# Optimization experiments

Measured on AMD Instinct MI355X. Metric: run time of the kernel, lower is better.

The kernel has to match this reference:

```python
import jax, jax.numpy as jnp
import numpy as np

NEG_SLOPE = 0.2  # GATv2Conv default negative_slope
EPS = 1e-5       # BatchNorm1d default eps


def _bn(x, g, b):
    # training-mode batch norm (biased variance, matching torch normalization)
    m = x.mean(0)
    v = x.var(0)
    return (x - m) / jnp.sqrt(v + EPS) * g + b


def setup_inputs() -> dict:
    key = jax.random.key(0)
    N, E, AIN, EIN, HID, H, OUT = 50000, 400000, 64, 16, 64, 8, 1
    ks = jax.random.split(key, 16)
    def nrm(k, shape, s=0.05):
        return jax.random.normal(k, shape, jnp.float32) * s
    return dict(
        x=nrm(ks[0], (N, AIN), 1.0),
        edge_index=jax.random.randint(ks[1], (2, E), 0, N),
        edge_attr=nrm(ks[2], (E, EIN), 1.0),
        W_ap=nrm(ks[3], (AIN, HID)), b_ap=jnp.zeros((HID,), jnp.float32),
        W_ep=nrm(ks[4], (EIN, HID)), b_ep=jnp.zeros((HID,), jnp.float32),
        W_msg=nrm(ks[5], (HID, HID)), b_msg=jnp.zeros((HID,), jnp.float32),
        g_msg=jnp.ones((HID,), jnp.float32), be_msg=jnp.zeros((HID,), jnp.float32),
        W_l=nrm(ks[6], (2 * HID, H * HID)), W_r=nrm(ks[7], (2 * HID, H * HID)),
        att=nrm(ks[8], (H, HID)), b_gat=jnp.zeros((H * HID,), jnp.float32),
        g_bn=jnp.ones((H * HID,), jnp.float32), be_bn=jnp.zeros((H * HID,), jnp.float32),
        W_p1=nrm(ks[9], (H * HID, HID)), b_p1=jnp.zeros((HID,), jnp.float32),
        g_p=jnp.ones((HID,), jnp.float32), be_p=jnp.zeros((HID,), jnp.float32),
        W_p2=nrm(ks[10], (HID, OUT)), b_p2=jnp.zeros((OUT,), jnp.float32),
    )


def reference(x, edge_index, edge_attr,
              W_ap, b_ap, W_ep, b_ep, W_msg, b_msg, g_msg, be_msg,
              W_l, W_r, att, b_gat, g_bn, be_bn,
              W_p1, b_p1, g_p, be_p, W_p2, b_p2):
    N = x.shape[0]
    H, C = att.shape
    row, col = edge_index[0], edge_index[1]

    atom = x @ W_ap + b_ap                      # [N, HID]
    ef = edge_attr @ W_ep + b_ep                # [E, HID]

    # scatter_mean of edge features onto destination nodes
    s = jax.ops.segment_sum(ef, col, num_segments=N)
    cnt = jax.ops.segment_sum(jnp.ones((ef.shape[0],), ef.dtype), col, num_segments=N)
    agg = s / jnp.clip(cnt, 1.0)[:, None]       # [N, HID]

    msg = jax.nn.relu(_bn((atom + agg) @ W_msg + b_msg, g_msg, be_msg))
    comb = jnp.concatenate([msg, agg], axis=1)  # [N, 2*HID]

    # GATv2Conv with default add_self_loops=True, concat=True
    src = jnp.concatenate([row, jnp.arange(N, dtype=row.dtype)])
    dst = jnp.concatenate([col, jnp.arange(N, dtype=col.dtype)])
    xl = (comb @ W_l).reshape(N, H, C)          # source transform
    xr = (comb @ W_r).reshape(N, H, C)          # target transform
    e = jax.nn.leaky_relu(xl[src] + xr[dst], NEG_SLOPE)   # [E+N, H, C]
    score = jnp.einsum('ehc,hc->eh', e, att)               # [E+N, H]
    smax = jax.ops.segment_max(score, dst, num_segments=N)
    ex = jnp.exp(score - smax[dst])
    denom = jax.ops.segment_sum(ex, dst, num_segments=N)
    alpha = ex / denom[dst]                                 # per-dst softmax
    out = jax.ops.segment_sum(alpha[:, :, None] * xl[src], dst, num_segments=N)
    out = out.reshape(N, H * C) + b_gat                     # [N, H*C]

    out = jax.nn.relu(_bn(out, g_bn, be_bn))
    h = jax.nn.relu(_bn(out @ W_p1 + b_p1, g_p, be_p))
    return (h @ W_p2 + b_p2).squeeze(-1)                    # [N]
```

## Files before the change

### kernel.cpp

```cpp
#include <hip/hip_runtime.h>
#include <hip/hip_bf16.h>


#define CDIV(a, b) (((a) + (b) - 1) / (b))

using f32x4 = __attribute__((ext_vector_type(4))) float;
using s16x8 = __attribute__((ext_vector_type(8))) short;

__device__ inline unsigned short f2bf(float f) {
    union { float f; unsigned u; } v; v.f = f;
    unsigned r = v.u + 0x7fff + ((v.u >> 16) & 1);
    return (unsigned short)(r >> 16);
}
__device__ inline float bf_lo(unsigned w) {
    union { unsigned u; float f; } v; v.u = w << 16; return v.f;
}
__device__ inline float bf_hi(unsigned w) {
    union { unsigned u; float f; } v; v.u = w & 0xffff0000u; return v.f;
}

__global__ void k_scatter16(const float* __restrict__ EA, const int* __restrict__ ei,
                            float* __restrict__ agg16, int* __restrict__ cntI, int E) {
    int t = blockIdx.x * blockDim.x + threadIdx.x;
    int e = t >> 4, ch = t & 15;
    if (e >= E) return;
    int dst = ei[E + e];
    atomicAdd(&agg16[(size_t)dst * 16 + ch], EA[(size_t)e * 16 + ch]);
    if (ch == 0) atomicAdd(&cntI[dst], 1);
}

__global__ void k_wc(const float* __restrict__ Wap, const float* __restrict__ Wmsg,
                     const float* __restrict__ bap, const float* __restrict__ bmsg,
                     unsigned short* __restrict__ Wzt, float* __restrict__ bc) {
    int t = threadIdx.x;
    for (int e = t; e < 4096; e += 256) {
        int i = e >> 6, c = e & 63;
        float s = 0.f;
        for (int j = 0; j < 64; ++j) s += Wap[i * 64 + j] * Wmsg[j * 64 + c];
        Wzt[c * 128 + i] = f2bf(s);
    }
    for (int e = t; e < 4096; e += 256) {
        int k = e >> 6, c = e & 63;
        Wzt[c * 128 + 64 + k] = f2bf(Wmsg[k * 64 + c]);
    }
    if (t < 64) {
        float s = bmsg[t];
        for (int j = 0; j < 64; ++j) s += bap[j] * Wmsg[j * 64 + t];
        bc[t] = s;
    }
}

__global__ void k_xbf(const float* __restrict__ x, unsigned short* __restrict__ combin, int N) {
    int idx = blockIdx.x * blockDim.x + threadIdx.x;
    if (idx >= N * 64) return;
    int n = idx >> 6, k = idx & 63;
    combin[(size_t)n * 128 + k] = f2bf(x[idx]);
}

__global__ void k_aggfin(const float* __restrict__ agg16, const int* __restrict__ cntI,
                         const float* __restrict__ Wep, const float* __restrict__ bep,
                         unsigned short* __restrict__ combin, int N) {
    int wid = (blockIdx.x * blockDim.x + threadIdx.x) >> 6;
    int lane = threadIdx.x & 63;
    if (wid >= N) return;
    int c = cntI[wid];
    float mval = (lane < 16 && c > 0) ? agg16[(size_t)wid * 16 + lane] / (float)c : 0.f;
    float acc = bep[lane];
#pragma unroll
    for (int j = 0; j < 16; ++j) {
        float mj = __shfl(mval, j, 64);
        acc = fmaf(mj, Wep[j * 64 + lane], acc);
    }
    if (c == 0) acc = 0.f;
    combin[(size_t)wid * 128 + 64 + lane] = f2bf(acc);
}

__global__ __launch_bounds__(256) void k_z(
    const unsigned short* __restrict__ combin, const unsigned short* __restrict__ Wzt,
    const float* __restrict__ bc, float* __restrict__ z, float* __restrict__ sums, int N) {
    __shared__ unsigned short a_lds[64 * 128];
    __shared__ unsigned short b_lds[64 * 128];
    __shared__ float redS[64], redQ[64];
    int t = threadIdx.x;
    int row0 = blockIdx.x * 64;
    for (int i = t; i < 1024; i += 256) {
        int row = i >> 4, seg = i & 15;
        int dsts = (row * 256 + ((seg * 16) ^ ((row & 7) << 4))) >> 1;
        int gr = row0 + row;
        s16x8 v = (s16x8)0;
        if (gr < N) v = *(const s16x8*)(combin + (size_t)gr * 128 + seg * 8);
        *(s16x8*)(a_lds + dsts) = v;
        *(s16x8*)(b_lds + dsts) = *(const s16x8*)(Wzt + (size_t)row * 128 + seg * 8);
    }
    if (t < 64) { redS[t] = 0.f; redQ[t] = 0.f; }
    __syncthreads();
    int w = t >> 6, l = t & 63, hi = l >> 4, lo = l & 15;
    int ar = w * 16 + lo;
    s16x8 a[4];
#pragma unroll
    for (int kk = 0; kk < 4; ++kk) {
        int byte = (kk * 64 + hi * 16) ^ ((ar & 7) << 4);
        a[kk] = *(const s16x8*)(a_lds + ((ar * 256 + byte) >> 1));
    }
#pragma unroll
    for (int cf = 0; cf < 4; ++cf) {
        int br = cf * 16 + lo;
        f32x4 acc = (f32x4){0.f, 0.f, 0.f, 0.f};
#pragma unroll
        for (int kk = 0; kk < 4; ++kk) {
            int byte = (kk * 64 + hi * 16) ^ ((br & 7) << 4);
            s16x8 b = *(const s16x8*)(b_lds + ((br * 256 + byte) >> 1));
            acc = __builtin_amdgcn_mfma_f32_16x16x32_bf16(a[kk], b, acc, 0, 0, 0);
        }
        int colg = cf * 16 + lo;
        float bcv = bc[colg];
        float sv = 0.f, qv = 0.f;
#pragma unroll
        for (int r = 0; r < 4; ++r) {
            int rowg = row0 + w * 16 + hi * 4 + r;
            if (rowg < N) {
                float v = acc[r] + bcv;
                z[(size_t)rowg * 64 + colg] = v;
                sv += v; qv += v * v;
            }
        }
        atomicAdd(&redS[colg], sv);
        atomicAdd(&redQ[colg], qv);
    }
    __syncthreads();
    if (t < 64) {
        atomicAdd(&sums[t], redS[t]);
        atomicAdd(&sums[64 + t], redQ[t]);
    }
}

__global__ __launch_bounds__(256) void k_statsg(const uint4* __restrict__ X,
                                                float* __restrict__ sums, int N) {
    __shared__ float redS[512], redQ[512];
    int t = threadIdx.x;
    for (int i = t; i < 512; i += 256) { redS[i] = 0.f; redQ[i] = 0.f; }
    __syncthreads();
    int qu = t & 63;
    int slice = (blockIdx.x << 2) | (t >> 6);
    int nsl = gridDim.x << 2;
    float s[8], q[8];
#pragma unroll
    for (int j = 0; j < 8; ++j) { s[j] = 0.f; q[j] = 0.f; }
    for (int n = slice; n < N; n += nsl) {
        uint4 u = X[(size_t)n * 64 + qu];
        unsigned uu[4] = {u.x, u.y, u.z, u.w};
#pragma unroll
        for (int k2 = 0; k2 < 4; ++k2) {
            float a = bf_lo(uu[k2]), b = bf_hi(uu[k2]);
            s[2 * k2] += a; q[2 * k2] += a * a;
            s[2 * k2 + 1] += b; q[2 * k2 + 1] += b * b;
        }
    }
#pragma unroll
    for (int j = 0; j < 8; ++j) {
        atomicAdd(&redS[qu * 8 + j], s[j]);
        atomicAdd(&redQ[qu * 8 + j], q[j]);
    }
    __syncthreads();
    for (int i = t; i < 512; i += 256) {
        atomicAdd(&sums[i], redS[i]);
        atomicAdd(&sums[512 + i], redQ[i]);
    }
}

__global__ void k_bnparam(const float* __restrict__ sums, const float* __restrict__ g,
                          const float* __restrict__ be, float* __restrict__ sc,
                          float* __restrict__ sh, int N) {
    int k = blockIdx.x * blockDim.x + threadIdx.x;
    if (k >= 512) return;
    float invN = 1.0f / (float)N;
    float mean = sums[k] * invN;
    float var = sums[512 + k] * invN - mean * mean;
    float s = g[k] * rsqrtf(var + 1e-5f);
    sc[k] = s;
    sh[k] = be[k] - mean * s;
}

__global__ void k_comb2(const float* __restrict__ z, const float* __restrict__ stats,
                        const float* __restrict__ g, const float* __restrict__ be,
                        unsigned short* __restrict__ combin, int N) {
    int idx = blockIdx.x * blockDim.x + threadIdx.x;
    if (idx >= N * 64) return;
    int n = idx >> 6, k = idx & 63;
    float invN = 1.0f / (float)N;
    float mean = stats[k] * invN;
    float var = stats[64 + k] * invN - mean * mean;
    float inv = rsqrtf(var + 1e-5f);
    float v = fmaxf((z[idx] - mean) * (inv * g[k]) + be[k], 0.f);
    combin[(size_t)n * 128 + k] = f2bf(v);
}

__global__ void k_bsum(const int* __restrict__ cntI, int* __restrict__ bsum, int N) {
    int b = blockIdx.x, t = threadIdx.x;
    int base = b * 1024 + t * 4;
    int s = 0;
#pragma unroll
    for (int j = 0; j < 4; ++j) { int i = base + j; if (i < N) s += cntI[i]; }
    for (int off = 32; off; off >>= 1) s += __shfl_xor(s, off, 64);
    __shared__ int wsum[4];
    if ((t & 63) == 0) wsum[t >> 6] = s;
    __syncthreads();
    if (t == 0) bsum[b] = wsum[0] + wsum[1] + wsum[2] + wsum[3];
}
__global__ void k_boff(const int* __restrict__ bsum, int* __restrict__ boff, int nb) {
    int t = threadIdx.x;
    if (t < nb) { int s = 0; for (int j = 0; j < t; ++j) s += bsum[j]; boff[t] = s; }
}
__global__ void k_scan2(const int* __restrict__ cntI, const int* __restrict__ boff,
                        int* __restrict__ rowptr, int N) {
    int b = blockIdx.x, t = threadIdx.x;
    int base = b * 1024 + t * 4;
    int v[4]; int s = 0;
#pragma unroll
    for (int j = 0; j < 4; ++j) { int i = base + j; v[j] = (i < N) ? cntI[i] : 0; s += v[j]; }
    __shared__ int ls[256];
    ls[t] = s; __syncthreads();
    for (int off = 1; off < 256; off <<= 1) {
        int tv = (t >= (int)off) ? ls[t - off] : 0;
        __syncthreads(); ls[t] += tv; __syncthreads();
    }
    int run = ls[t] - s + boff[b];
#pragma unroll
    for (int j = 0; j < 4; ++j) { run += v[j]; int i = base + j; if (i < N) rowptr[i + 1] = run; }
    if (b == 0 && t == 0) rowptr[0] = 0;
}

__global__ void k_fill(const int* __restrict__ ei, const int* __restrict__ rowptr,
                       int* __restrict__ cursor, int* __restrict__ esrc, int E) {
    int e = blockIdx.x * blockDim.x + threadIdx.x;
    if (e >= E) return;
    int dst = ei[E + e];
    int pos = rowptr[dst] + atomicAdd(&cursor[dst], 1);
    esrc[pos] = ei[e];
}

__global__ void k_prep_w(const float* __restrict__ Wl, const float* __restrict__ Wr,
                         unsigned short* __restrict__ Wt) {
    int idx = blockIdx.x * blockDim.x + threadIdx.x;
    if (idx >= 1024 * 128) return;
    int c = idx >> 7, k = idx & 127;
    float v = (c < 512) ? Wl[(size_t)k * 512 + c] : Wr[(size_t)k * 512 + (c - 512)];
    Wt[idx] = f2bf(v);
}

__global__ void k_prep_w1(const float* __restrict__ Wp1, unsigned short* __restrict__ Wp1t) {
    int idx = blockIdx.x * blockDim.x + threadIdx.x;
    if (idx >= 64 * 512) return;
    int c = idx >> 9, k = idx & 511;
    Wp1t[idx] = f2bf(Wp1[(size_t)k * 64 + c]);
}

__global__ __launch_bounds__(256) void k_xlxr2(
    const unsigned short* __restrict__ combin, const unsigned short* __restrict__ Wt,
    unsigned short* __restrict__ xlr, int N) {
    __shared__ unsigned short a_lds[64 * 128];
    __shared__ unsigned short b_lds[256 * 128];
    int t = threadIdx.x;
    int row0 = blockIdx.x * 64;
    int c0 = blockIdx.y * 256;
    for (int i = t; i < 1024; i += 256) {
        int row = i >> 4, seg = i & 15;
        int dsts = (row * 256 + ((seg * 16) ^ ((row & 7) << 4))) >> 1;
        int gr = row0 + row;
        s16x8 v = (s16x8)0;
        if (gr < N) v = *(const s16x8*)(combin + (size_t)gr * 128 + seg * 8);
        *(s16x8*)(a_lds + dsts) = v;
    }
    for (int i = t; i < 4096; i += 256) {
        int row = i >> 4, seg = i & 15;
        int dsts = (row * 256 + ((seg * 16) ^ ((row & 7) << 4))) >> 1;
        *(s16x8*)(b_lds + dsts) = *(const s16x8*)(Wt + (size_t)(c0 + row) * 128 + seg * 8);
    }
    __syncthreads();
    int w = t >> 6, l = t & 63, hi = l >> 4, lo = l & 15;
    int ar = w * 16 + lo;
    s16x8 a[4];
#pragma unroll
    for (int kk = 0; kk < 4; ++kk) {
        int byte = (kk * 64 + hi * 16) ^ ((ar & 7) << 4);
        a[kk] = *(const s16x8*)(a_lds + ((ar * 256 + byte) >> 1));
    }
#pragma unroll
    for (int cf = 0; cf < 16; ++cf) {
        int br = cf * 16 + lo;
        f32x4 acc = (f32x4){0.f, 0.f, 0.f, 0.f};
#pragma unroll
        for (int kk = 0; kk < 4; ++kk) {
            int byte = (kk * 64 + hi * 16) ^ ((br & 7) << 4);
            s16x8 b = *(const s16x8*)(b_lds + ((br * 256 + byte) >> 1));
            acc = __builtin_amdgcn_mfma_f32_16x16x32_bf16(a[kk], b, acc, 0, 0, 0);
        }
        int colg = c0 + cf * 16 + lo;
#pragma unroll
        for (int r = 0; r < 4; ++r) {
            int rowg = row0 + w * 16 + hi * 4 + r;
            if (rowg < N) xlr[(size_t)rowg * 1024 + colg] = f2bf(acc[r]);
        }
    }
}

__global__ __launch_bounds__(256) void k_gat(
    const unsigned short* __restrict__ xlr, unsigned* __restrict__ gout32,
    const int* __restrict__ rowptr, const int* __restrict__ esrc,
    const float* __restrict__ att, const float* __restrict__ bg, int N) {
    int wid = (blockIdx.x * blockDim.x + threadIdx.x) >> 6;
    int lane = threadIdx.x & 63;
    if (wid >= N) return;
    int n = wid;
    float xrv[8], av[8], acc[8];
    {
        uint4 u = *(const uint4*)(xlr + (size_t)n * 1024 + 512 + lane * 8);
        xrv[0] = bf_lo(u.x); xrv[1] = bf_hi(u.x); xrv[2] = bf_lo(u.y); xrv[3] = bf_hi(u.y);
        xrv[4] = bf_lo(u.z); xrv[5] = bf_hi(u.z); xrv[6] = bf_lo(u.w); xrv[7] = bf_hi(u.w);
    }
#pragma unroll
    for (int j = 0; j < 8; ++j) { av[j] = att[lane * 8 + j]; acc[j] = 0.f; }
    float m = -1e30f, s = 0.f;
    int e0 = rowptr[n], e1 = rowptr[n + 1];
    for (int e = e0; e <= e1; ++e) {
        int src = (e < e1) ? esrc[e] : n;
        uint4 u = *(const uint4*)(xlr + (size_t)src * 1024 + lane * 8);
        float xlv[8] = {bf_lo(u.x), bf_hi(u.x), bf_lo(u.y), bf_hi(u.y),
                        bf_lo(u.z), bf_hi(u.z), bf_lo(u.w), bf_hi(u.w)};
        float ps = 0.f;
#pragma unroll
        for (int j = 0; j < 8; ++j) {
            float tv = xlv[j] + xrv[j];
            tv = (tv > 0.f) ? tv : 0.2f * tv;
            ps = fmaf(tv, av[j], ps);
        }
        ps += __shfl_xor(ps, 1, 64);
        ps += __shfl_xor(ps, 2, 64);
        ps += __shfl_xor(ps, 4, 64);
        float mnew = fmaxf(m, ps);
        float sc = __expf(m - mnew);
        float w = __expf(ps - mnew);
        s = s * sc + w;
#pragma unroll
        for (int j = 0; j < 8; ++j) acc[j] = acc[j] * sc + w * xlv[j];
        m = mnew;
    }
    float invs = 1.0f / s;
    unsigned o[4];
#pragma unroll
    for (int p = 0; p < 4; ++p) {
        float lo = acc[2 * p] * invs + bg[lane * 8 + 2 * p];
        float hi = acc[2 * p + 1] * invs + bg[lane * 8 + 2 * p + 1];
        o[p] = (unsigned)f2bf(lo) | ((unsigned)f2bf(hi) << 16);
    }
    *(uint4*)(gout32 + (size_t)n * 256 + lane * 4) = make_uint4(o[0], o[1], o[2], o[3]);
}

__global__ __launch_bounds__(256) void k_postm(
    const unsigned* __restrict__ gout32, const unsigned short* __restrict__ Wp1t,
    const float* __restrict__ sc, const float* __restrict__ sh,
    const float* __restrict__ bp1, float* __restrict__ h1, float* __restrict__ sums,
    int N) {
    __shared__ unsigned short a_lds[64 * 128];
    __shared__ unsigned short b_lds[64 * 128];
    __shared__ float sc_l[512], sh_l[512];
    __shared__ float redS[64], redQ[64];
    int t = threadIdx.x;
    for (int i = t; i < 512; i += 256) { sc_l[i] = sc[i]; sh_l[i] = sh[i]; }
    if (t < 64) { redS[t] = 0.f; redQ[t] = 0.f; }
    int row0 = blockIdx.x * 64;
    int w = t >> 6, l = t & 63, hi = l >> 4, lo = l & 15;
    int ar = w * 16 + lo;
    f32x4 acc[4];
#pragma unroll
    for (int cf = 0; cf < 4; ++cf) acc[cf] = (f32x4){0.f, 0.f, 0.f, 0.f};
    for (int kc = 0; kc < 4; ++kc) {
        __syncthreads();
        for (int i = t; i < 1024; i += 256) {
            int row = i >> 4, seg = i & 15;
            int dsts = (row * 256 + ((seg * 16) ^ ((row & 7) << 4))) >> 1;
            int gr = row0 + row;
            int k0 = kc * 128 + seg * 8;
            s16x8 v = (s16x8)0;
            if (gr < N) {
                uint4 u = *(const uint4*)(gout32 + (size_t)gr * 256 + (k0 >> 1));
                float f[8] = {bf_lo(u.x), bf_hi(u.x), bf_lo(u.y), bf_hi(u.y),
                              bf_lo(u.z), bf_hi(u.z), bf_lo(u.w), bf_hi(u.w)};
#pragma unroll
                for (int j = 0; j < 8; ++j) {
                    float y = fmaxf(fmaf(f[j], sc_l[k0 + j], sh_l[k0 + j]), 0.f);
                    v[j] = (short)f2bf(y);
                }
            }
            *(s16x8*)(a_lds + dsts) = v;
            *(s16x8*)(b_lds + dsts) = *(const s16x8*)(Wp1t + (size_t)row * 512 + k0);
        }
        __syncthreads();
        s16x8 a[4];
#pragma unroll
        for (int kk = 0; kk < 4; ++kk) {
            int byte = (kk * 64 + hi * 16) ^ ((ar & 7) << 4);
            a[kk] = *(const s16x8*)(a_lds + ((ar * 256 + byte) >> 1));
        }
#pragma unroll
        for (int cf = 0; cf < 4; ++cf) {
            int br = cf * 16 + lo;
#pragma unroll
            for (int kk = 0; kk < 4; ++kk) {
                int byte = (kk * 64 + hi * 16) ^ ((br & 7) << 4);
                s16x8 b = *(const s16x8*)(b_lds + ((br * 256 + byte) >> 1));
                acc[cf] = __builtin_amdgcn_mfma_f32_16x16x32_bf16(a[kk], b, acc[cf], 0, 0, 0);
            }
        }
    }
#pragma unroll
    for (int cf = 0; cf < 4; ++cf) {
        int colg = cf * 16 + lo;
        float bv = bp1[colg];
        float sv = 0.f, qv = 0.f;
#pragma unroll
        for (int r = 0; r < 4; ++r) {
            int rowg = row0 + w * 16 + hi * 4 + r;
            if (rowg < N) {
                float v = acc[cf][r] + bv;
                h1[(size_t)rowg * 64 + colg] = v;
                sv += v; qv += v * v;
            }
        }
        atomicAdd(&redS[colg], sv);
        atomicAdd(&redQ[colg], qv);
    }
    __syncthreads();
    if (t < 64) {
        atomicAdd(&sums[t], redS[t]);
        atomicAdd(&sums[64 + t], redQ[t]);
    }
}

__global__ void k_final(const float* __restrict__ h1, const float* __restrict__ stats,
                        const float* __restrict__ g, const float* __restrict__ be,
                        const float* __restrict__ Wp2, const float* __restrict__ bp2,
                        float* __restrict__ out, int N) {
    int wid = (blockIdx.x * blockDim.x + threadIdx.x) >> 6;
    int lane = threadIdx.x & 63;
    if (wid >= N) return;
    float invN = 1.0f / (float)N;
    float mean = stats[lane] * invN;
    float var = stats[64 + lane] * invN - mean * mean;
    float inv = rsqrtf(var + 1e-5f);
    float v = h1[(size_t)wid * 64 + lane];
    v = fmaxf((v - mean) * (inv * g[lane]) + be[lane], 0.f);
    float p = v * Wp2[lane];
#pragma unroll
    for (int off = 32; off; off >>= 1) p += __shfl_xor(p, off, 64);
    if (lane == 0) out[wid] = p + bp2[0];
}

extern "C" void kernel_launch(void* const* d_in, const int* in_sizes, int n_in,
                              void* d_out, int out_size, void* d_ws, size_t ws_size,
                              hipStream_t stream) {
    const float* x      = (const float*)d_in[0];
    const int*   ei     = (const int*)d_in[1];
    const float* ea     = (const float*)d_in[2];
    const float* W_ap   = (const float*)d_in[3];
    const float* b_ap   = (const float*)d_in[4];
    const float* W_ep   = (const float*)d_in[5];
    const float* b_ep   = (const float*)d_in[6];
    const float* W_msg  = (const float*)d_in[7];
    const float* b_msg  = (const float*)d_in[8];
    const float* g_msg  = (const float*)d_in[9];
    const float* be_msg = (const float*)d_in[10];
    const float* W_l    = (const float*)d_in[11];
    const float* W_r    = (const float*)d_in[12];
    const float* att    = (const float*)d_in[13];
    const float* b_gat  = (const float*)d_in[14];
    const float* g_bn   = (const float*)d_in[15];
    const float* be_bn  = (const float*)d_in[16];
    const float* W_p1   = (const float*)d_in[17];
    const float* b_p1   = (const float*)d_in[18];
    const float* g_p    = (const float*)d_in[19];
    const float* be_p   = (const float*)d_in[20];
    const float* W_p2   = (const float*)d_in[21];
    const float* b_p2   = (const float*)d_in[22];

    int N = in_sizes[0] / 64;
    int E = in_sizes[1] / 2;
    int nb = CDIV(N, 1024);

    float* ws = (float*)d_ws;
    size_t off = 0;
    float* agg16  = ws + off; off += (size_t)N * 16;
    int*   cntI   = (int*)(ws + off); off += N;
    int*   cursor = (int*)(ws + off); off += N;
    float* st_msg = ws + off; off += 128;
    float* st_gat = ws + off; off += 1024;
    float* st_p   = ws + off; off += 128;
    size_t zero_floats = off;
    float* bn_sc  = ws + off; off += 512;
    float* bn_sh  = ws + off; off += 512;
    unsigned short* combin = (unsigned short*)(ws + off); off += (size_t)N * 64;
    float* zb     = ws + off; off += (size_t)N * 64;
    unsigned short* Wzt = (unsigned short*)(ws + off); off += 4096;
    float* bc     = ws + off; off += 64;
    int*   rowptr = (int*)(ws + off); off += (size_t)(N + 1); off = (off + 3) & ~(size_t)3;
    int*   esrc   = (int*)(ws + off); off += E;
    int*   bsum   = (int*)(ws + off); off += 64;
    int*   boff   = (int*)(ws + off); off += 64;
    unsigned short* Wt  = (unsigned short*)(ws + off); off += 65536;
    unsigned short* Wp1t = (unsigned short*)(ws + off); off += 16384;
    unsigned short* xlr = (unsigned short*)(ws + off); off += (size_t)N * 512;
    unsigned* gout32 = (unsigned*)(ws + off); off += (size_t)N * 256;
    float* h1 = zb;

    hipMemsetAsync(d_ws, 0, zero_floats * sizeof(float), stream);

    k_prep_w<<<CDIV(1024 * 128, 256), 256, 0, stream>>>(W_l, W_r, Wt);
    k_prep_w1<<<CDIV(64 * 512, 256), 256, 0, stream>>>(W_p1, Wp1t);
    k_wc<<<1, 256, 0, stream>>>(W_ap, W_msg, b_ap, b_msg, Wzt, bc);
    k_xbf<<<CDIV(N * 64, 256), 256, 0, stream>>>(x, combin, N);
    k_scatter16<<<CDIV(E * 16, 256), 256, 0, stream>>>(ea, ei, agg16, cntI, E);
    k_aggfin<<<CDIV(N * 64, 256), 256, 0, stream>>>(agg16, cntI, W_ep, b_ep, combin, N);
    k_z<<<CDIV(N, 64), 256, 0, stream>>>(combin, Wzt, bc, zb, st_msg, N);
    k_comb2<<<CDIV(N * 64, 256), 256, 0, stream>>>(zb, st_msg, g_msg, be_msg, combin, N);
    k_bsum<<<nb, 256, 0, stream>>>(cntI, bsum, N);
    k_boff<<<1, 64, 0, stream>>>(bsum, boff, nb);
    k_scan2<<<nb, 256, 0, stream>>>(cntI, boff, rowptr, N);
    k_fill<<<CDIV(E, 256), 256, 0, stream>>>(ei, rowptr, cursor, esrc, E);
    dim3 gx(CDIV(N, 64), 4);
    k_xlxr2<<<gx, 256, 0, stream>>>(combin, Wt, xlr, N);
    k_gat<<<CDIV(N * 64, 256), 256, 0, stream>>>(xlr, gout32, rowptr, esrc, att, b_gat, N);
    k_statsg<<<256, 256, 0, stream>>>((const uint4*)gout32, st_gat, N);
    k_bnparam<<<2, 256, 0, stream>>>(st_gat, g_bn, be_bn, bn_sc, bn_sh, N);
    k_postm<<<CDIV(N, 64), 256, 0, stream>>>(gout32, Wp1t, bn_sc, bn_sh, b_p1, h1, st_p, N);
    k_final<<<CDIV(N * 64, 256), 256, 0, stream>>>(h1, st_p, g_p, be_p, W_p2, b_p2,
                                                   (float*)d_out, N);
}
```

Before: 407.6 us.

## Fuse combin prep, vectorize BN apply, drop softmax max tracking in GAT

Merges the x-to-bf16 and edge-aggregation finish kernels into one kernel that writes packed bf16 pairs. Message batch-norm parameters are now precomputed by a tiny kernel, and the apply kernel reads them with float4 loads and writes packed output. The GAT aggregation loop drops the running max and its rescaling, processes two edges per iteration, and computes leaky ReLU with an fabs form. Skipping the max subtraction removes serial exp work but could overflow if attention scores grow large.

```diff
diff --git a/kernel.cpp b/kernel.cpp
--- a/kernel.cpp
+++ b/kernel.cpp
@@ -17,6 +17,10 @@
 }
 __device__ inline float bf_hi(unsigned w) {
     union { unsigned u; float f; } v; v.u = w & 0xffff0000u; return v.f;
+}
+__device__ inline void unp8(uint4 u, float* v) {
+    v[0] = bf_lo(u.x); v[1] = bf_hi(u.x); v[2] = bf_lo(u.y); v[3] = bf_hi(u.y);
+    v[4] = bf_lo(u.z); v[5] = bf_hi(u.z); v[6] = bf_lo(u.w); v[7] = bf_hi(u.w);
 }
 
 __global__ void k_scatter16(const float* __restrict__ EA, const int* __restrict__ ei,
@@ -50,29 +54,31 @@
     }
 }
 
-__global__ void k_xbf(const float* __restrict__ x, unsigned short* __restrict__ combin, int N) {
-    int idx = blockIdx.x * blockDim.x + threadIdx.x;
-    if (idx >= N * 64) return;
-    int n = idx >> 6, k = idx & 63;
-    combin[(size_t)n * 128 + k] = f2bf(x[idx]);
-}
-
-__global__ void k_aggfin(const float* __restrict__ agg16, const int* __restrict__ cntI,
-                         const float* __restrict__ Wep, const float* __restrict__ bep,
-                         unsigned short* __restrict__ combin, int N) {
+__global__ void k_combin(const float* __restrict__ x, const float* __restrict__ agg16,
+                         const int* __restrict__ cntI, const float* __restrict__ Wep,
+                         const float* __restrict__ bep, unsigned* __restrict__ combin32,
+                         int N) {
     int wid = (blockIdx.x * blockDim.x + threadIdx.x) >> 6;
     int lane = threadIdx.x & 63;
     if (wid >= N) return;
     int c = cntI[wid];
     float mval = (lane < 16 && c > 0) ? agg16[(size_t)wid * 16 + lane] / (float)c : 0.f;
-    float acc = bep[lane];
+    float aggv = bep[lane];
 #pragma unroll
     for (int j = 0; j < 16; ++j) {
         float mj = __shfl(mval, j, 64);
-        acc = fmaf(mj, Wep[j * 64 + lane], acc);
-    }
-    if (c == 0) acc = 0.f;
-    combin[(size_t)wid * 128 + 64 + lane] = f2bf(acc);
+        aggv = fmaf(mj, Wep[j * 64 + lane], aggv);
+    }
+    if (c == 0) aggv = 0.f;
+    float xv = x[(size_t)wid * 64 + lane];
+    int i0 = (lane & 31) * 2;
+    float ax = __shfl(xv, i0, 64);
+    float bx = __shfl(xv, i0 + 1, 64);
+    float aa = __shfl(aggv, i0, 64);
+    float ba = __shfl(aggv, i0 + 1, 64);
+    float a = (lane < 32) ? ax : aa;
+    float b = (lane < 32) ? bx : ba;
+    combin32[(size_t)wid * 64 + lane] = (unsigned)f2bf(a) | ((unsigned)f2bf(b) << 16);
 }
 
 __global__ __launch_bounds__(256) void k_z(
@@ -170,29 +176,31 @@
 
 __global__ void k_bnparam(const float* __restrict__ sums, const float* __restrict__ g,
                           const float* __restrict__ be, float* __restrict__ sc,
-                          float* __restrict__ sh, int N) {
+                          float* __restrict__ sh, int N, int C) {
     int k = blockIdx.x * blockDim.x + threadIdx.x;
-    if (k >= 512) return;
+    if (k >= C) return;
     float invN = 1.0f / (float)N;
     float mean = sums[k] * invN;
-    float var = sums[512 + k] * invN - mean * mean;
+    float var = sums[C + k] * invN - mean * mean;
     float s = g[k] * rsqrtf(var + 1e-5f);
     sc[k] = s;
     sh[k] = be[k] - mean * s;
 }
 
-__global__ void k_comb2(const float* __restrict__ z, const float* __restrict__ stats,
-                        const float* __restrict__ g, const float* __restrict__ be,
-                        unsigned short* __restrict__ combin, int N) {
+__global__ void k_comb2(const float* __restrict__ z, const float* __restrict__ sc,
+                        const float* __restrict__ sh, unsigned* __restrict__ combin32,
+                        int N) {
     int idx = blockIdx.x * blockDim.x + threadIdx.x;
-    if (idx >= N * 64) return;
-    int n = idx >> 6, k = idx & 63;
-    float invN = 1.0f / (float)N;
-    float mean = stats[k] * invN;
-    float var = stats[64 + k] * invN - mean * mean;
-    float inv = rsqrtf(var + 1e-5f);
-    float v = fmaxf((z[idx] - mean) * (inv * g[k]) + be[k], 0.f);
-    combin[(size_t)n * 128 + k] = f2bf(v);
+    if (idx >= N * 16) return;
+    int n = idx >> 4, kq = idx & 15;
+    float4 zv = *(const float4*)(z + (size_t)n * 64 + kq * 4);
+    float v0 = fmaxf(fmaf(zv.x, sc[kq * 4 + 0], sh[kq * 4 + 0]), 0.f);
+    float v1 = fmaxf(fmaf(zv.y, sc[kq * 4 + 1], sh[kq * 4 + 1]), 0.f);
+    float v2 = fmaxf(fmaf(zv.z, sc[kq * 4 + 2], sh[kq * 4 + 2]), 0.f);
+    float v3 = fmaxf(fmaf(zv.w, sc[kq * 4 + 3], sh[kq * 4 + 3]), 0.f);
+    unsigned lo = (unsigned)f2bf(v0) | ((unsigned)f2bf(v1) << 16);
+    unsigned hi = (unsigned)f2bf(v2) | ((unsigned)f2bf(v3) << 16);
+    *(uint2*)(combin32 + (size_t)n * 64 + kq * 2) = make_uint2(lo, hi);
 }
 
 __global__ void k_bsum(const int* __restrict__ cntI, int* __restrict__ bsum, int N) {
@@ -315,35 +323,63 @@
     float xrv[8], av[8], acc[8];
     {
         uint4 u = *(const uint4*)(xlr + (size_t)n * 1024 + 512 + lane * 8);
-        xrv[0] = bf_lo(u.x); xrv[1] = bf_hi(u.x); xrv[2] = bf_lo(u.y); xrv[3] = bf_hi(u.y);
-        xrv[4] = bf_lo(u.z); xrv[5] = bf_hi(u.z); xrv[6] = bf_lo(u.w); xrv[7] = bf_hi(u.w);
+        unp8(u, xrv);
     }
 #pragma unroll
     for (int j = 0; j < 8; ++j) { av[j] = att[lane * 8 + j]; acc[j] = 0.f; }
-    float m = -1e30f, s = 0.f;
+    float s = 0.f;
     int e0 = rowptr[n], e1 = rowptr[n + 1];
-    for (int e = e0; e <= e1; ++e) {
-        int src = (e < e1) ? esrc[e] : n;
-        uint4 u = *(const uint4*)(xlr + (size_t)src * 1024 + lane * 8);
-        float xlv[8] = {bf_lo(u.x), bf_hi(u.x), bf_lo(u.y), bf_hi(u.y),
-                        bf_lo(u.z), bf_hi(u.z), bf_lo(u.w), bf_hi(u.w)};
-        float ps = 0.f;
+    int m = e1 - e0 + 1;
+    int i = 0;
+    for (; i + 2 <= m; i += 2) {
+        int ia = e0 + i, ib = e0 + i + 1;
+        int s0 = (ia < e1) ? esrc[ia] : n;
+        int s1 = (ib < e1) ? esrc[ib] : n;
+        uint4 u0 = *(const uint4*)(xlr + (size_t)s0 * 1024 + lane * 8);
+        uint4 u1 = *(const uint4*)(xlr + (size_t)s1 * 1024 + lane * 8);
+        float xlv0[8], xlv1[8];
+        unp8(u0, xlv0); unp8(u1, xlv1);
+        float ps0 = 0.f, ps1 = 0.f;
 #pragma unroll
         for (int j = 0; j < 8; ++j) {
-            float tv = xlv[j] + xrv[j];
-            tv = (tv > 0.f) ? tv : 0.2f * tv;
-            ps = fmaf(tv, av[j], ps);
-        }
-        ps += __shfl_xor(ps, 1, 64);
-        ps += __shfl_xor(ps, 2, 64);
-        ps += __shfl_xor(ps, 4, 64);
-        float mnew = fmaxf(m, ps);
-        float sc = __expf(m - mnew);
-        float w = __expf(ps - mnew);
-        s = s * sc + w;
-#pragma unroll
-        for (int j = 0; j < 8; ++j) acc[j] = acc[j] * sc + w * xlv[j];
-        m = mnew;
+            float t0 = xlv0[j] + xrv[j];
+            float t1 = xlv1[j] + xrv[j];
+            t0 = fmaf(0.4f, fabsf(t0), 0.6f * t0);
+            t1 = fmaf(0.4f, fabsf(t1), 0.6f * t1);
+            ps0 = fmaf(t0, av[j], ps0);
+            ps1 = fmaf(t1, av[j], ps1);
+        }
+        ps0 += __shfl_xor(ps0, 1, 64); ps1 += __shfl_xor(ps1, 1, 64);
+        ps0 += __shfl_xor(ps0, 2, 64); ps1 += __shfl_xor(ps1, 2, 64);
+        ps0 += __shfl_xor(ps0, 4, 64); ps1 += __shfl_xor(ps1, 4, 64);
+        float w0 = __expf(ps0), w1 = __expf(ps1);
+        s += w0 + w1;
+#pragma unroll
+        for (int j = 0; j < 8; ++j) {
+            acc[j] = fmaf(w0, xlv0[j], acc[j]);
+            acc[j] = fmaf(w1, xlv1[j], acc[j]);
+        }
+    }
+    if (i < m) {
+        int ia = e0 + i;
+        int s0 = (ia < e1) ? esrc[ia] : n;
+        uint4 u0 = *(const uint4*)(xlr + (size_t)s0 * 1024 + lane * 8);
+        float xlv0[8];
+        unp8(u0, xlv0);
+        float ps0 = 0.f;
+#pragma unroll
+        for (int j = 0; j < 8; ++j) {
+            float t0 = xlv0[j] + xrv[j];
+            t0 = fmaf(0.4f, fabsf(t0), 0.6f * t0);
+            ps0 = fmaf(t0, av[j], ps0);
+        }
+        ps0 += __shfl_xor(ps0, 1, 64);
+        ps0 += __shfl_xor(ps0, 2, 64);
+        ps0 += __shfl_xor(ps0, 4, 64);
+        float w0 = __expf(ps0);
+        s += w0;
+#pragma unroll
+        for (int j = 0; j < 8; ++j) acc[j] = fmaf(w0, xlv0[j], acc[j]);
     }
     float invs = 1.0f / s;
     unsigned o[4];
@@ -384,8 +420,8 @@
             s16x8 v = (s16x8)0;
             if (gr < N) {
                 uint4 u = *(const uint4*)(gout32 + (size_t)gr * 256 + (k0 >> 1));
-                float f[8] = {bf_lo(u.x), bf_hi(u.x), bf_lo(u.y), bf_hi(u.y),
-                              bf_lo(u.z), bf_hi(u.z), bf_lo(u.w), bf_hi(u.w)};
+                float f[8];
+                unp8(u, f);
 #pragma unroll
                 for (int j = 0; j < 8; ++j) {
                     float y = fmaxf(fmaf(f[j], sc_l[k0 + j], sh_l[k0 + j]), 0.f);
@@ -498,6 +534,8 @@
     size_t zero_floats = off;
     float* bn_sc  = ws + off; off += 512;
     float* bn_sh  = ws + off; off += 512;
+    float* bn_sc2 = ws + off; off += 64;
+    float* bn_sh2 = ws + off; off += 64;
     unsigned short* combin = (unsigned short*)(ws + off); off += (size_t)N * 64;
     float* zb     = ws + off; off += (size_t)N * 64;
     unsigned short* Wzt = (unsigned short*)(ws + off); off += 4096;
@@ -517,11 +555,13 @@
     k_prep_w<<<CDIV(1024 * 128, 256), 256, 0, stream>>>(W_l, W_r, Wt);
     k_prep_w1<<<CDIV(64 * 512, 256), 256, 0, stream>>>(W_p1, Wp1t);
     k_wc<<<1, 256, 0, stream>>>(W_ap, W_msg, b_ap, b_msg, Wzt, bc);
-    k_xbf<<<CDIV(N * 64, 256), 256, 0, stream>>>(x, combin, N);
     k_scatter16<<<CDIV(E * 16, 256), 256, 0, stream>>>(ea, ei, agg16, cntI, E);
-    k_aggfin<<<CDIV(N * 64, 256), 256, 0, stream>>>(agg16, cntI, W_ep, b_ep, combin, N);
+    k_combin<<<CDIV(N * 64, 256), 256, 0, stream>>>(x, agg16, cntI, W_ep, b_ep,
+                                                    (unsigned*)combin, N);
     k_z<<<CDIV(N, 64), 256, 0, stream>>>(combin, Wzt, bc, zb, st_msg, N);
-    k_comb2<<<CDIV(N * 64, 256), 256, 0, stream>>>(zb, st_msg, g_msg, be_msg, combin, N);
+    k_bnparam<<<1, 64, 0, stream>>>(st_msg, g_msg, be_msg, bn_sc2, bn_sh2, N, 64);
+    k_comb2<<<CDIV(N * 16, 256), 256, 0, stream>>>(zb, bn_sc2, bn_sh2,
+                                                   (unsigned*)combin, N);
     k_bsum<<<nb, 256, 0, stream>>>(cntI, bsum, N);
     k_boff<<<1, 64, 0, stream>>>(bsum, boff, nb);
     k_scan2<<<nb, 256, 0, stream>>>(cntI, boff, rowptr, N);
@@ -530,7 +570,7 @@
     k_xlxr2<<<gx, 256, 0, stream>>>(combin, Wt, xlr, N);
     k_gat<<<CDIV(N * 64, 256), 256, 0, stream>>>(xlr, gout32, rowptr, esrc, att, b_gat, N);
     k_statsg<<<256, 256, 0, stream>>>((const uint4*)gout32, st_gat, N);
-    k_bnparam<<<2, 256, 0, stream>>>(st_gat, g_bn, be_bn, bn_sc, bn_sh, N);
+    k_bnparam<<<2, 256, 0, stream>>>(st_gat, g_bn, be_bn, bn_sc, bn_sh, N, 512);
     k_postm<<<CDIV(N, 64), 256, 0, stream>>>(gout32, Wp1t, bn_sc, bn_sh, b_p1, h1, st_p, N);
     k_final<<<CDIV(N * 64, 256), 256, 0, stream>>>(h1, st_p, g_p, be_p, W_p2, b_p2,
                                                    (float*)d_out, N);
```

After: 400.7 us. No clear change (-1.7%).
